# Kernel optimization log

Measured on AMD Instinct MI355X. Metric: run time of the kernel, lower is better.

Reference implementation:

```python
import jax, jax.numpy as jnp
import numpy as np

D = 8  # sheaf block size


def setup_inputs() -> dict:
    key = jax.random.key(0)
    k1, k2, k3 = jax.random.split(key, 3)
    n, e = 1024, 32768
    x = jax.random.normal(k1, (n, D), dtype=jnp.float32)
    edge_index = jax.random.randint(k2, (2, e), 0, n, dtype=jnp.int64)
    # Phi: PyG MLP(num_layers=1, bias=False) == Linear(D, D*D, bias=False), weight [out, in]
    W = jax.random.normal(k3, (D * D, D), dtype=jnp.float32) * (1.0 / np.sqrt(D))
    return {"x": x, "edge_index": edge_index, "W": W}


def reference(x, edge_index, W):
    src, dst = edge_index[0], edge_index[1]
    # sym=True branch: |x_i - x_j| per edge  -> [e, D]
    x_in = jnp.abs(x[src] - x[dst])
    # single linear layer, no bias -> [e, D*D] -> [e, D, D]
    R_tmp = (x_in @ W.T).reshape(-1, D, D)
    n = x.shape[0]
    # dense n x n x D x D output; torch uses empty + indexed assign, we use zeros + scatter-set
    R = jnp.zeros((n, n, D, D), dtype=x.dtype).at[src, dst].set(R_tmp)
    return R
```

## Files before the change

### kernel.cpp

```cpp
#include <hip/hip_runtime.h>

#define D 8


__global__ void zero_ws_kernel(int* __restrict__ ws, int ntiles) {
    int i = blockIdx.x * blockDim.x + threadIdx.x;
    if (i < ntiles) ws[i] = 0;
}

__global__ void claim_ws_kernel(const int* __restrict__ src,
                                const int* __restrict__ dst,
                                int* __restrict__ ws, int n, int e) {
    int k = blockIdx.x * blockDim.x + threadIdx.x;
    if (k >= e) return;
    atomicMax(&ws[src[k] * n + dst[k]], k + 1);
}

__global__ void fused_out_kernel(const float* __restrict__ x,
                                 const int* __restrict__ src,
                                 const int* __restrict__ dst,
                                 const float* __restrict__ W,
                                 const int* __restrict__ ws,
                                 float4* __restrict__ out4,
                                 int ntiles) {
    int gid = blockIdx.x * blockDim.x + threadIdx.x;
    int tile = gid >> 4;
    int t = gid & 15;
    if (tile >= ntiles) return;

    int claim = ws[tile];
    if (claim == 0) {
        out4[gid] = make_float4(0.f, 0.f, 0.f, 0.f);
        return;
    }
    int k = claim - 1;
    int s = src[k], d = dst[k];
    const float* xs = x + s * D;
    const float* xd = x + d * D;

    float diff[D];
#pragma unroll
    for (int i = 0; i < D; ++i) diff[i] = fabsf(xs[i] - xd[i]);

    float4 r;
    float acc[4];
#pragma unroll
    for (int j = 0; j < 4; ++j) {
        int o = t * 4 + j;
        const float* w = W + o * D;
        float a = 0.f;
#pragma unroll
        for (int i = 0; i < D; ++i) a += diff[i] * w[i];
        acc[j] = a;
    }
    r.x = acc[0]; r.y = acc[1]; r.z = acc[2]; r.w = acc[3];
    out4[gid] = r;
}


__global__ void zero_out_kernel(float4* __restrict__ out4, int n4) {
    int i = blockIdx.x * blockDim.x + threadIdx.x;
    if (i < n4) out4[i] = make_float4(0.f, 0.f, 0.f, 0.f);
}

__global__ void claim_out_kernel(const int* __restrict__ src,
                                 const int* __restrict__ dst,
                                 int* __restrict__ out_i, int n, int e) {
    int k = blockIdx.x * blockDim.x + threadIdx.x;
    if (k >= e) return;
    long long pair = (long long)src[k] * n + dst[k];
    atomicMax(&out_i[pair * 64], k + 1);
}

__global__ void scatter_out_kernel(const float* __restrict__ x,
                                   const int* __restrict__ src,
                                   const int* __restrict__ dst,
                                   const float* __restrict__ W,
                                   float* __restrict__ out, int n, int e) {
    int gid = blockIdx.x * blockDim.x + threadIdx.x;
    int k = gid >> 6;
    int o = gid & 63;
    if (k >= e) return;
    int s = src[k], d = dst[k];
    long long base = ((long long)s * n + d) * 64;
    int claim = __float_as_int(out[base]);
    if (claim != k + 1) return;
    const float* xs = x + s * D;
    const float* xd = x + d * D;
    const float* w = W + o * D;
    float a = 0.f;
#pragma unroll
    for (int i = 0; i < D; ++i) a += fabsf(xs[i] - xd[i]) * w[i];
    out[base + o] = a;
}

extern "C" void kernel_launch(void* const* d_in, const int* in_sizes, int n_in,
                              void* d_out, int out_size, void* d_ws, size_t ws_size,
                              hipStream_t stream) {
    const float* x  = (const float*)d_in[0];
    const int*   ei = (const int*)d_in[1];
    const float* W  = (const float*)d_in[2];

    int n = in_sizes[0] / D;
    int e = in_sizes[1] / 2;
    const int* src = ei;
    const int* dst = ei + e;

    int ntiles = out_size / 64;
    int n4 = out_size / 4;

    if (ws_size >= (size_t)ntiles * sizeof(int)) {
        int* ws = (int*)d_ws;
        {
            int threads = 256, blocks = (ntiles + threads - 1) / threads;
            zero_ws_kernel<<<blocks, threads, 0, stream>>>(ws, ntiles);
        }
        {
            int threads = 256, blocks = (e + threads - 1) / threads;
            claim_ws_kernel<<<blocks, threads, 0, stream>>>(src, dst, ws, n, e);
        }
        {
            int threads = 256;
            long long total = (long long)ntiles * 16;
            int blocks = (int)((total + threads - 1) / threads);
            fused_out_kernel<<<blocks, threads, 0, stream>>>(
                x, src, dst, W, ws, (float4*)d_out, ntiles);
        }
    } else {
        {
            int threads = 256, blocks = (n4 + threads - 1) / threads;
            zero_out_kernel<<<blocks, threads, 0, stream>>>((float4*)d_out, n4);
        }
        {
            int threads = 256, blocks = (e + threads - 1) / threads;
            claim_out_kernel<<<blocks, threads, 0, stream>>>(src, dst, (int*)d_out, n, e);
        }
        {
            int threads = 256;
            long long total = (long long)e * 64;
            int blocks = (int)((total + threads - 1) / threads);
            scatter_out_kernel<<<blocks, threads, 0, stream>>>(
                x, src, dst, W, (float*)d_out, n, e);
        }
    }
}
```

Measured before the change: 258.8 us.

## Zero output with memset and scatter only claimed edges instead of dense tile pass

Replaces the dense per-tile pass that wrote zeros or computed blocks for every output tile with a hipMemsetAsync of the whole output plus an edge-parallel kernel that writes only the winning edge's block. The workspace zeroing also moves to hipMemsetAsync. This removes the per-tile workspace lookups and lets the runtime's fill path handle the bulk zero write. In exchange, claimed tiles are written twice and the stores become scattered rather than streaming.

```diff
diff --git a/kernel.cpp b/kernel.cpp
--- a/kernel.cpp
+++ b/kernel.cpp
@@ -3,10 +3,6 @@
 #define D 8
 
 
-__global__ void zero_ws_kernel(int* __restrict__ ws, int ntiles) {
-    int i = blockIdx.x * blockDim.x + threadIdx.x;
-    if (i < ntiles) ws[i] = 0;
-}
 
 __global__ void claim_ws_kernel(const int* __restrict__ src,
                                 const int* __restrict__ dst,
@@ -16,33 +12,27 @@
     atomicMax(&ws[src[k] * n + dst[k]], k + 1);
 }
 
-__global__ void fused_out_kernel(const float* __restrict__ x,
-                                 const int* __restrict__ src,
-                                 const int* __restrict__ dst,
-                                 const float* __restrict__ W,
-                                 const int* __restrict__ ws,
-                                 float4* __restrict__ out4,
-                                 int ntiles) {
+__global__ void scatter_claimed_kernel(const float* __restrict__ x,
+                                       const int* __restrict__ src,
+                                       const int* __restrict__ dst,
+                                       const float* __restrict__ W,
+                                       const int* __restrict__ ws,
+                                       float4* __restrict__ out4,
+                                       int n, int e) {
     int gid = blockIdx.x * blockDim.x + threadIdx.x;
-    int tile = gid >> 4;
+    int k = gid >> 4;
     int t = gid & 15;
-    if (tile >= ntiles) return;
+    if (k >= e) return;
+    int s = src[k], d = dst[k];
+    int tile = s * n + d;
+    if (ws[tile] != k + 1) return;
 
-    int claim = ws[tile];
-    if (claim == 0) {
-        out4[gid] = make_float4(0.f, 0.f, 0.f, 0.f);
-        return;
-    }
-    int k = claim - 1;
-    int s = src[k], d = dst[k];
     const float* xs = x + s * D;
     const float* xd = x + d * D;
-
     float diff[D];
 #pragma unroll
     for (int i = 0; i < D; ++i) diff[i] = fabsf(xs[i] - xd[i]);
 
-    float4 r;
     float acc[4];
 #pragma unroll
     for (int j = 0; j < 4; ++j) {
@@ -53,15 +43,11 @@
         for (int i = 0; i < D; ++i) a += diff[i] * w[i];
         acc[j] = a;
     }
+    float4 r;
     r.x = acc[0]; r.y = acc[1]; r.z = acc[2]; r.w = acc[3];
-    out4[gid] = r;
+    out4[(size_t)tile * 16 + t] = r;
 }
 
-
-__global__ void zero_out_kernel(float4* __restrict__ out4, int n4) {
-    int i = blockIdx.x * blockDim.x + threadIdx.x;
-    if (i < n4) out4[i] = make_float4(0.f, 0.f, 0.f, 0.f);
-}
 
 __global__ void claim_out_kernel(const int* __restrict__ src,
                                  const int* __restrict__ dst,
@@ -107,30 +93,25 @@
     const int* dst = ei + e;
 
     int ntiles = out_size / 64;
-    int n4 = out_size / 4;
+    size_t out_bytes = (size_t)out_size * sizeof(float);
 
     if (ws_size >= (size_t)ntiles * sizeof(int)) {
         int* ws = (int*)d_ws;
-        {
-            int threads = 256, blocks = (ntiles + threads - 1) / threads;
-            zero_ws_kernel<<<blocks, threads, 0, stream>>>(ws, ntiles);
-        }
+        hipMemsetAsync(d_out, 0, out_bytes, stream);
+        hipMemsetAsync(ws, 0, (size_t)ntiles * sizeof(int), stream);
         {
             int threads = 256, blocks = (e + threads - 1) / threads;
             claim_ws_kernel<<<blocks, threads, 0, stream>>>(src, dst, ws, n, e);
         }
         {
             int threads = 256;
-            long long total = (long long)ntiles * 16;
-            int blocks = (int)((total + threads - 1) / threads);
-            fused_out_kernel<<<blocks, threads, 0, stream>>>(
-                x, src, dst, W, ws, (float4*)d_out, ntiles);
+            int total = e * 16;
+            int blocks = (total + threads - 1) / threads;
+            scatter_claimed_kernel<<<blocks, threads, 0, stream>>>(
+                x, src, dst, W, ws, (float4*)d_out, n, e);
         }
     } else {
-        {
-            int threads = 256, blocks = (n4 + threads - 1) / threads;
-            zero_out_kernel<<<blocks, threads, 0, stream>>>((float4*)d_out, n4);
-        }
+        hipMemsetAsync(d_out, 0, out_bytes, stream);
         {
             int threads = 256, blocks = (e + threads - 1) / threads;
             claim_out_kernel<<<blocks, threads, 0, stream>>>(src, dst, (int*)d_out, n, e);
```

Measured after the change: 269.4 us. 1.04x slower.
